# Optimization experiments

Hardware: AMD Instinct MI355X
Metric: run time of the kernel (lower is better)

Reference implementation:

```python
import jax, jax.numpy as jnp
import numpy as np

B, C, N = 16, 64, 2048
K, KS, OC = 20, 20, 64
BN_EPS = 1e-5


def setup_inputs() -> dict:
    key = jax.random.key(0)
    k1, k2, k3, k4 = jax.random.split(key, 4)
    feature = jax.random.normal(k1, (B, C, N), dtype=jnp.float32)
    neigh_indexs = jax.random.randint(k2, (B * N, K), 0, B * N, dtype=jnp.int64)
    permatrix = jax.random.normal(k3, (B * N, K, KS), dtype=jnp.float32)
    conv_w = jax.random.normal(k4, (OC, 2 * C), dtype=jnp.float32) * 0.05  # 1x1 conv weight
    conv_b = jnp.zeros((OC,), dtype=jnp.float32)
    gamma = jnp.ones((OC,), dtype=jnp.float32)
    beta = jnp.zeros((OC,), dtype=jnp.float32)
    return {"feature": feature, "neigh_indexs": neigh_indexs, "permatrix": permatrix,
            "conv_w": conv_w, "conv_b": conv_b, "gamma": gamma, "beta": beta}


def _forward(feature, neigh_indexs, permatrix, conv_w, conv_b, gamma, beta):
    bsize, num_feat, num_pts = feature.shape
    # [B, C, N] -> [B*N, C]
    flat = jnp.transpose(feature, (0, 2, 1)).reshape(bsize * num_pts, num_feat)
    # neighbor gather: [B*N, K, C] -> [B*N, C, K]
    feats = jnp.transpose(flat[neigh_indexs], (0, 2, 1))
    f_repeat = jnp.broadcast_to(feats[:, :, 0:1], feats.shape)
    f_relative = feats - f_repeat
    feats = jnp.concatenate([f_repeat, f_relative], axis=1)  # [B*N, 2C, K]
    # per-point small matmul with permutation matrix: [B*N, 2C, KS]
    feats = jnp.einsum('nck,nks->ncs', feats, permatrix)
    # 1x1 conv over channel dim: [B*N, OC, KS]
    out = jnp.einsum('ncs,oc->nos', feats, conv_w) + conv_b[None, :, None]
    # max over neighbors, reshape to [B, OC, N]
    out = jnp.max(out, axis=-1).reshape(bsize, num_pts, -1)
    out = jnp.transpose(out, (0, 2, 1))  # [B, OC, N]
    # BatchNorm1d (training-mode forward: biased var over batch & points)
    mean = jnp.mean(out, axis=(0, 2), keepdims=True)
    var = jnp.var(out, axis=(0, 2), keepdims=True)
    out = (out - mean) * jax.lax.rsqrt(var + BN_EPS)
    return out * gamma[None, :, None] + beta[None, :, None]


def reference(feature, neigh_indexs, permatrix, conv_w, conv_b, gamma, beta):
    return _forward(feature, neigh_indexs, permatrix, conv_w, conv_b, gamma, beta)
```

## Files before the change

kernel.cpp:

```cpp
#include <hip/hip_runtime.h>

#define B_   16
#define C_   64
#define N_   2048
#define M_   (B_ * N_)
#define K_   20
#define KS_  20
#define OC_  64
#define NWAVE2 8192
#define NBLK2  2048

__global__ __launch_bounds__(256) void k_project(
    const float* __restrict__ feat,
    const float* __restrict__ conv_w,
    float* __restrict__ pq)
{
    const int lane = threadIdx.x & 63;
    const int wg   = blockIdx.x * 4 + (threadIdx.x >> 6);
    float w2[64], wd[64];
    const float4* cw4 = (const float4*)conv_w;
    #pragma unroll
    for (int j = 0; j < 16; ++j) {
        float4 a = cw4[lane * 32 + j];
        float4 b = cw4[lane * 32 + 16 + j];
        w2[4*j+0] = b.x; w2[4*j+1] = b.y; w2[4*j+2] = b.z; w2[4*j+3] = b.w;
        wd[4*j+0] = a.x - b.x; wd[4*j+1] = a.y - b.y;
        wd[4*j+2] = a.z - b.z; wd[4*j+3] = a.w - b.w;
    }
    const int m0 = wg * 16;
    int b0 = m0 >> 11, p0 = m0 & 2047;
    float fv = feat[((size_t)(b0 * 64 + lane)) * 2048 + p0];
    for (int mi = 0; mi < 16; ++mi) {
        const int m = m0 + mi;
        float fnext = 0.f;
        if (mi < 15) {
            const int mn = m + 1;
            fnext = feat[((size_t)((mn >> 11) * 64 + lane)) * 2048 + (mn & 2047)];
        }
        float p0a = 0.f, p1a = 0.f, q0a = 0.f, q1a = 0.f;
        #pragma unroll
        for (int c = 0; c < 32; ++c) {
            float f0 = __int_as_float(
                __builtin_amdgcn_readlane(__float_as_int(fv), c));
            float f1 = __int_as_float(
                __builtin_amdgcn_readlane(__float_as_int(fv), c + 32));
            p0a = fmaf(w2[c], f0, p0a);
            p1a = fmaf(w2[c + 32], f1, p1a);
            q0a = fmaf(wd[c], f0, q0a);
            q1a = fmaf(wd[c + 32], f1, q1a);
        }
        pq[(size_t)m * 128 + lane]      = p0a + p1a;
        pq[(size_t)m * 128 + 64 + lane] = q0a + q1a;
        fv = fnext;
    }
}

template<int E>
__device__ __forceinline__ float bro(const float4& pa, const float4& pb) {
    constexpr int c = E & 3;
    float v;
    if constexpr (E < 256) {
        if constexpr (c == 0) v = pa.x; else if constexpr (c == 1) v = pa.y;
        else if constexpr (c == 2) v = pa.z; else v = pa.w;
    } else {
        if constexpr (c == 0) v = pb.x; else if constexpr (c == 1) v = pb.y;
        else if constexpr (c == 2) v = pb.z; else v = pb.w;
    }
    constexpr int l = (E < 256) ? (E >> 2) : ((E >> 2) - 64);
    return __int_as_float(__builtin_amdgcn_readlane(__float_as_int(v), l));
}

#define KS1(K,S) acc[S] = fmaf(t, bro<(K)*20+(S)>(pa, pb), acc[S]);
#define KSTEP(K) { const float t = pk[K] + q; \
    KS1(K,0)  KS1(K,1)  KS1(K,2)  KS1(K,3)  KS1(K,4)  \
    KS1(K,5)  KS1(K,6)  KS1(K,7)  KS1(K,8)  KS1(K,9)  \
    KS1(K,10) KS1(K,11) KS1(K,12) KS1(K,13) KS1(K,14) \
    KS1(K,15) KS1(K,16) KS1(K,17) KS1(K,18) KS1(K,19) }

template<bool PREF>
__device__ __forceinline__ void point_step(
    int n, int lane, float bias, int& iv,
    float4& pa, float4& pb, float4& npa, float4& npb,
    const float* __restrict__ pq, const int* __restrict__ nidx,
    const float* __restrict__ perm,
    float* __restrict__ pre, float& sum, float& sumsq)
{
    int ik[20];
    #pragma unroll
    for (int k = 0; k < 20; ++k) ik[k] = __builtin_amdgcn_readlane(iv, k);
    float q = pq[(size_t)ik[0] * 128 + 64 + lane];
    float pk[20];
    #pragma unroll
    for (int k = 0; k < 20; ++k) pk[k] = pq[(size_t)ik[k] * 128 + lane];
    if (PREF) {
        const int nn = n + NWAVE2;
        if (lane < 20) iv = nidx[(size_t)nn * K_ + lane];
        const float* src = perm + (size_t)nn * 400;
        npa = *(const float4*)(src + lane * 4);
        if (lane < 36) npb = *(const float4*)(src + 256 + lane * 4);
    }

    float acc[20];
    #pragma unroll
    for (int s = 0; s < 20; ++s) acc[s] = bias;
    KSTEP(0)  KSTEP(1)  KSTEP(2)  KSTEP(3)  KSTEP(4)
    KSTEP(5)  KSTEP(6)  KSTEP(7)  KSTEP(8)  KSTEP(9)
    KSTEP(10) KSTEP(11) KSTEP(12) KSTEP(13) KSTEP(14)
    KSTEP(15) KSTEP(16) KSTEP(17) KSTEP(18) KSTEP(19)

    float mv = acc[0];
    #pragma unroll
    for (int s = 1; s < 20; ++s) mv = fmaxf(mv, acc[s]);
    pre[(size_t)n * 64 + lane] = mv;
    sum += mv;
    sumsq = fmaf(mv, mv, sumsq);
}

__global__ __launch_bounds__(256) void k_points(
    const float* __restrict__ pq,
    const int*   __restrict__ nidx,
    const float* __restrict__ perm,
    const float* __restrict__ conv_b,
    float* __restrict__ pre,
    float* __restrict__ partials)
{
    const int tid  = threadIdx.x;
    const int lane = tid & 63;
    const int w    = tid >> 6;
    const int wg   = (int)blockIdx.x * 4 + w;

    const float bias = conv_b[lane];
    float sum = 0.f, sumsq = 0.f;

    float4 pa, pb, npa, npb;
    int iv = 0;
    {
        const float* src = perm + (size_t)wg * 400;
        pa = *(const float4*)(src + lane * 4);
        if (lane < 36) pb = *(const float4*)(src + 256 + lane * 4);
        if (lane < 20) iv = nidx[(size_t)wg * K_ + lane];
    }

    point_step<true >(wg,              lane, bias, iv, pa,  pb,  npa, npb,
                      pq, nidx, perm, pre, sum, sumsq);
    point_step<true >(wg + NWAVE2,     lane, bias, iv, npa, npb, pa,  pb,
                      pq, nidx, perm, pre, sum, sumsq);
    point_step<true >(wg + 2 * NWAVE2, lane, bias, iv, pa,  pb,  npa, npb,
                      pq, nidx, perm, pre, sum, sumsq);
    point_step<false>(wg + 3 * NWAVE2, lane, bias, iv, npa, npb, pa,  pb,
                      pq, nidx, perm, pre, sum, sumsq);

    __shared__ float red[512];
    red[w * 128 + lane]      = sum;
    red[w * 128 + 64 + lane] = sumsq;
    __syncthreads();
    if (tid < 128) {
        float s = red[tid] + red[128 + tid] + red[256 + tid] + red[384 + tid];
        partials[(size_t)blockIdx.x * 128 + tid] = s;
    }
}

#undef KSTEP
#undef KS1

__global__ __launch_bounds__(256) void k_stats(
    const float* __restrict__ partials,
    const float* __restrict__ gamma,
    const float* __restrict__ beta,
    float* __restrict__ stats)
{
    const int ch  = blockIdx.x;
    const int tid = threadIdx.x;
    double s = 0.0, s2 = 0.0;
    for (int w = tid; w < NBLK2; w += 256) {
        s  += (double)partials[(size_t)w * 128 + ch];
        s2 += (double)partials[(size_t)w * 128 + 64 + ch];
    }
    __shared__ double sh_s[256];
    __shared__ double sh_q[256];
    sh_s[tid] = s; sh_q[tid] = s2;
    __syncthreads();
    for (int off = 128; off > 0; off >>= 1) {
        if (tid < off) { sh_s[tid] += sh_s[tid + off]; sh_q[tid] += sh_q[tid + off]; }
        __syncthreads();
    }
    if (tid == 0) {
        const double inv_n = 1.0 / (double)M_;
        double mean = sh_s[0] * inv_n;
        double var  = sh_q[0] * inv_n - mean * mean;
        double inv  = 1.0 / sqrt(var + 1e-5);
        double sc   = (double)gamma[ch] * inv;
        stats[ch]      = (float)sc;
        stats[64 + ch] = (float)((double)beta[ch] - mean * sc);
    }
}

__global__ __launch_bounds__(256) void k_apply(
    const float* __restrict__ pre,
    const float* __restrict__ stats,
    float* __restrict__ out)
{
    __shared__ float tile[64 * 65];
    __shared__ float scl[64];
    __shared__ float shf[64];
    const int tid = threadIdx.x;
    if (tid < 64)       scl[tid]      = stats[tid];
    else if (tid < 128) shf[tid - 64] = stats[tid];
    __syncthreads();
    const int b  = blockIdx.x >> 5;
    const int pt = (blockIdx.x & 31) * 64;
    const int c  = tid & 63;
    const int r0 = tid >> 6;
    #pragma unroll
    for (int i = 0; i < 16; ++i) {
        const int r = i * 4 + r0;
        float v = pre[((size_t)(b * 2048 + pt + r)) * 64 + c];
        tile[c * 65 + r] = fmaf(v, scl[c], shf[c]);
    }
    __syncthreads();
    #pragma unroll
    for (int i = 0; i < 16; ++i) {
        const int o = i * 4 + r0;
        out[((size_t)(b * 64 + o)) * 2048 + pt + c] = tile[o * 65 + c];
    }
}

extern "C" void kernel_launch(void* const* d_in, const int* in_sizes, int n_in,
                              void* d_out, int out_size, void* d_ws, size_t ws_size,
                              hipStream_t stream) {
    const float* feat   = (const float*)d_in[0];
    const int*   nidx   = (const int*)  d_in[1];
    const float* perm   = (const float*)d_in[2];
    const float* conv_w = (const float*)d_in[3];
    const float* conv_b = (const float*)d_in[4];
    const float* gamma  = (const float*)d_in[5];
    const float* beta   = (const float*)d_in[6];
    float* out = (float*)d_out;

    char* ws = (char*)d_ws;
    float* pq       = (float*)ws;
    float* pre      = (float*)(ws + (size_t)M_ * 128 * 4);
    float* partials = (float*)(ws + (size_t)M_ * 128 * 4
                                  + (size_t)M_ * 64 * 4);
    float* stats    = (float*)(ws + (size_t)M_ * 128 * 4
                                  + (size_t)M_ * 64 * 4
                                  + (size_t)NBLK2 * 128 * 4);

    hipLaunchKernelGGL(k_project, dim3(512),  dim3(256), 0, stream, feat, conv_w, pq);
    hipLaunchKernelGGL(k_points,  dim3(2048), dim3(256), 0, stream, pq, nidx, perm,
                       conv_b, pre, partials);
    hipLaunchKernelGGL(k_stats,   dim3(64),   dim3(256), 0, stream, partials, gamma,
                       beta, stats);
    hipLaunchKernelGGL(k_apply,   dim3(512),  dim3(256), 0, stream, pre, stats, out);
}
```

Before: 181.6 us.

## Double-buffer neighbor gathers one point ahead and preload all indices

The per-point loop is restructured so the full gather for the next point (the 20 projected neighbor rows, q, and the perm matrix) is issued before the current point is computed, using two Pt buffers. All four index vectors are loaded up front. The first k-step now initializes the accumulators from the bias directly, and launch bounds request 4 blocks per CU. This aims to hide gather latency better, at the cost of more live registers, which could force spills under the occupancy hint.

```diff
diff --git a/kernel.cpp b/kernel.cpp
--- a/kernel.cpp
+++ b/kernel.cpp
@@ -70,40 +70,44 @@
     return __int_as_float(__builtin_amdgcn_readlane(__float_as_int(v), l));
 }
 
+struct Pt { float4 pa, pb; float q; float pk[20]; };
+
+__device__ __forceinline__ void issue_point(
+    int n, int lane, int iv,
+    const float* __restrict__ pq, const float* __restrict__ perm, Pt& P)
+{
+    int ik[20];
+    #pragma unroll
+    for (int k = 0; k < 20; ++k) ik[k] = __builtin_amdgcn_readlane(iv, k);
+    P.q = pq[(size_t)ik[0] * 128 + 64 + lane];
+    #pragma unroll
+    for (int k = 0; k < 20; ++k) P.pk[k] = pq[(size_t)ik[k] * 128 + lane];
+    const float* src = perm + (size_t)n * 400;
+    P.pa = *(const float4*)(src + lane * 4);
+    if (lane < 36) P.pb = *(const float4*)(src + 256 + lane * 4);
+}
+
 #define KS1(K,S) acc[S] = fmaf(t, bro<(K)*20+(S)>(pa, pb), acc[S]);
-#define KSTEP(K) { const float t = pk[K] + q; \
+#define KSI(S)   acc[S] = fmaf(t, bro<S>(pa, pb), bias);
+#define KSTEP(K) { const float t = P.pk[K] + P.q; \
     KS1(K,0)  KS1(K,1)  KS1(K,2)  KS1(K,3)  KS1(K,4)  \
     KS1(K,5)  KS1(K,6)  KS1(K,7)  KS1(K,8)  KS1(K,9)  \
     KS1(K,10) KS1(K,11) KS1(K,12) KS1(K,13) KS1(K,14) \
     KS1(K,15) KS1(K,16) KS1(K,17) KS1(K,18) KS1(K,19) }
-
-template<bool PREF>
-__device__ __forceinline__ void point_step(
-    int n, int lane, float bias, int& iv,
-    float4& pa, float4& pb, float4& npa, float4& npb,
-    const float* __restrict__ pq, const int* __restrict__ nidx,
-    const float* __restrict__ perm,
+#define KSTEP0 { const float t = P.pk[0] + P.q; \
+    KSI(0)  KSI(1)  KSI(2)  KSI(3)  KSI(4)  \
+    KSI(5)  KSI(6)  KSI(7)  KSI(8)  KSI(9)  \
+    KSI(10) KSI(11) KSI(12) KSI(13) KSI(14) \
+    KSI(15) KSI(16) KSI(17) KSI(18) KSI(19) }
+
+__device__ __forceinline__ void compute_point(
+    int n, int lane, float bias, const Pt& P,
     float* __restrict__ pre, float& sum, float& sumsq)
 {
-    int ik[20];
-    #pragma unroll
-    for (int k = 0; k < 20; ++k) ik[k] = __builtin_amdgcn_readlane(iv, k);
-    float q = pq[(size_t)ik[0] * 128 + 64 + lane];
-    float pk[20];
-    #pragma unroll
-    for (int k = 0; k < 20; ++k) pk[k] = pq[(size_t)ik[k] * 128 + lane];
-    if (PREF) {
-        const int nn = n + NWAVE2;
-        if (lane < 20) iv = nidx[(size_t)nn * K_ + lane];
-        const float* src = perm + (size_t)nn * 400;
-        npa = *(const float4*)(src + lane * 4);
-        if (lane < 36) npb = *(const float4*)(src + 256 + lane * 4);
-    }
-
+    const float4 pa = P.pa, pb = P.pb;
     float acc[20];
-    #pragma unroll
-    for (int s = 0; s < 20; ++s) acc[s] = bias;
-    KSTEP(0)  KSTEP(1)  KSTEP(2)  KSTEP(3)  KSTEP(4)
+    KSTEP0
+    KSTEP(1)  KSTEP(2)  KSTEP(3)  KSTEP(4)
     KSTEP(5)  KSTEP(6)  KSTEP(7)  KSTEP(8)  KSTEP(9)
     KSTEP(10) KSTEP(11) KSTEP(12) KSTEP(13) KSTEP(14)
     KSTEP(15) KSTEP(16) KSTEP(17) KSTEP(18) KSTEP(19)
@@ -116,7 +120,7 @@
     sumsq = fmaf(mv, mv, sumsq);
 }
 
-__global__ __launch_bounds__(256) void k_points(
+__global__ __launch_bounds__(256, 4) void k_points(
     const float* __restrict__ pq,
     const int*   __restrict__ nidx,
     const float* __restrict__ perm,
@@ -132,23 +136,23 @@
     const float bias = conv_b[lane];
     float sum = 0.f, sumsq = 0.f;
 
-    float4 pa, pb, npa, npb;
-    int iv = 0;
-    {
-        const float* src = perm + (size_t)wg * 400;
-        pa = *(const float4*)(src + lane * 4);
-        if (lane < 36) pb = *(const float4*)(src + 256 + lane * 4);
-        if (lane < 20) iv = nidx[(size_t)wg * K_ + lane];
-    }
-
-    point_step<true >(wg,              lane, bias, iv, pa,  pb,  npa, npb,
-                      pq, nidx, perm, pre, sum, sumsq);
-    point_step<true >(wg + NWAVE2,     lane, bias, iv, npa, npb, pa,  pb,
-                      pq, nidx, perm, pre, sum, sumsq);
-    point_step<true >(wg + 2 * NWAVE2, lane, bias, iv, pa,  pb,  npa, npb,
-                      pq, nidx, perm, pre, sum, sumsq);
-    point_step<false>(wg + 3 * NWAVE2, lane, bias, iv, npa, npb, pa,  pb,
-                      pq, nidx, perm, pre, sum, sumsq);
+    int iv0 = 0, iv1 = 0, iv2 = 0, iv3 = 0;
+    if (lane < 20) {
+        iv0 = nidx[(size_t)wg * K_ + lane];
+        iv1 = nidx[(size_t)(wg +     NWAVE2) * K_ + lane];
+        iv2 = nidx[(size_t)(wg + 2 * NWAVE2) * K_ + lane];
+        iv3 = nidx[(size_t)(wg + 3 * NWAVE2) * K_ + lane];
+    }
+
+    Pt A, B;
+    issue_point(wg,                  lane, iv0, pq, perm, A);
+    issue_point(wg +     NWAVE2,     lane, iv1, pq, perm, B);
+    compute_point(wg,                lane, bias, A, pre, sum, sumsq);
+    issue_point(wg + 2 * NWAVE2,     lane, iv2, pq, perm, A);
+    compute_point(wg +     NWAVE2,   lane, bias, B, pre, sum, sumsq);
+    issue_point(wg + 3 * NWAVE2,     lane, iv3, pq, perm, B);
+    compute_point(wg + 2 * NWAVE2,   lane, bias, A, pre, sum, sumsq);
+    compute_point(wg + 3 * NWAVE2,   lane, bias, B, pre, sum, sumsq);
 
     __shared__ float red[512];
     red[w * 128 + lane]      = sum;
@@ -161,7 +165,9 @@
 }
 
 #undef KSTEP
+#undef KSTEP0
 #undef KS1
+#undef KSI
 
 __global__ __launch_bounds__(256) void k_stats(
     const float* __restrict__ partials,
```

After: 181.6 us. About the same (-0.0%).
